# Performance work log

Hardware: AMD Instinct MI355X
Metric: run time of the kernel (lower is better)

## Reference

```python
import jax, jax.numpy as jnp
import numpy as np

N = 50000
IN_CH = 128
HID = 256
HEADS = 8
HEAD_DIM = HID // HEADS
NUM_CLASSES = 2
E = 800000
NEG_SLOPE = 0.2  # PyG GATConv default leaky_relu slope


def gat_conv(x, edge_index, W, att_src, att_dst, bias):
    """PyG-style GATConv (concat=True, add_self_loops=True, eval mode).
    x: [N, HID]; edge_index: [2, E] (row 0 = source j, row 1 = target i).
    W: [HID, HEADS*HEAD_DIM]; att_src/att_dst: [HEADS, HEAD_DIM]; bias: [HEADS*HEAD_DIM].
    """
    loop = jnp.arange(N)
    src = jnp.concatenate([edge_index[0], loop])  # self-loops appended
    dst = jnp.concatenate([edge_index[1], loop])
    h = (x @ W).reshape(N, HEADS, HEAD_DIM)          # [N, H, D]
    a_src = jnp.einsum('nhd,hd->nh', h, att_src)     # [N, H]
    a_dst = jnp.einsum('nhd,hd->nh', h, att_dst)
    e = jax.nn.leaky_relu(a_src[src] + a_dst[dst], NEG_SLOPE)  # [E+N, H]
    # segment softmax over incoming edges of each target node
    m = jax.ops.segment_max(e, dst, num_segments=N)
    p = jnp.exp(e - m[dst])
    s = jax.ops.segment_sum(p, dst, num_segments=N)
    alpha = p / (s[dst] + 1e-16)                     # [E+N, H]
    msg = h[src] * alpha[:, :, None]                 # [E+N, H, D]
    out = jax.ops.segment_sum(msg, dst, num_segments=N)  # [N, H, D]
    return out.reshape(N, HEADS * HEAD_DIM) + bias


def setup_inputs() -> dict:
    key = jax.random.key(0)
    ks = jax.random.split(key, 24)
    g = lambda k, shape, fan_in: jax.random.normal(k, shape, dtype=jnp.float32) / np.sqrt(fan_in)
    inp = {}
    inp['x'] = jax.random.normal(ks[0], (N, IN_CH), dtype=jnp.float32)
    inp['tut_edge_index'] = jax.random.randint(ks[1], (2, E), 0, N)
    inp['tdt_edge_index'] = jax.random.randint(ks[2], (2, E), 0, N)
    inp['proj_W'] = g(ks[3], (IN_CH, HID), IN_CH)
    inp['proj_b'] = jnp.zeros((HID,), jnp.float32)
    # 2 GAT layers per meta-path, stacked on leading axis
    inp['tut_W'] = g(ks[4], (2, HID, HID), HID)
    inp['tut_asrc'] = g(ks[5], (2, HEADS, HEAD_DIM), HEAD_DIM)
    inp['tut_adst'] = g(ks[6], (2, HEADS, HEAD_DIM), HEAD_DIM)
    inp['tut_bias'] = jnp.zeros((2, HID), jnp.float32)
    inp['tdt_W'] = g(ks[7], (2, HID, HID), HID)
    inp['tdt_asrc'] = g(ks[8], (2, HEADS, HEAD_DIM), HEAD_DIM)
    inp['tdt_adst'] = g(ks[9], (2, HEADS, HEAD_DIM), HEAD_DIM)
    inp['tdt_bias'] = jnp.zeros((2, HID), jnp.float32)
    inp['sem_att'] = jnp.full((2,), 0.5, jnp.float32)
    inp['cls_W1'] = g(ks[10], (HID, HID // 2), HID)
    inp['cls_b1'] = jnp.zeros((HID // 2,), jnp.float32)
    inp['cls_W2'] = g(ks[11], (HID // 2, NUM_CLASSES), HID // 2)
    inp['cls_b2'] = jnp.zeros((NUM_CLASSES,), jnp.float32)
    return inp


def reference(x, tut_edge_index, tdt_edge_index, proj_W, proj_b,
              tut_W, tut_asrc, tut_adst, tut_bias,
              tdt_W, tdt_asrc, tdt_adst, tdt_bias,
              sem_att, cls_W1, cls_b1, cls_W2, cls_b2):
    h = x @ proj_W + proj_b
    # TUT branch: 2 GATConv layers (eval mode -> dropout is identity)
    h_tut = h
    for l in range(2):
        h_tut = gat_conv(h_tut, tut_edge_index, tut_W[l], tut_asrc[l], tut_adst[l], tut_bias[l])
        h_tut = jax.nn.elu(h_tut)
    # TDT branch
    h_tdt = h
    for l in range(2):
        h_tdt = gat_conv(h_tdt, tdt_edge_index, tdt_W[l], tdt_asrc[l], tdt_adst[l], tdt_bias[l])
        h_tdt = jax.nn.elu(h_tdt)
    w = jax.nn.softmax(sem_att)
    z = w[0] * h_tut + w[1] * h_tdt
    hc = jax.nn.relu(z @ cls_W1 + cls_b1)
    logits = hc @ cls_W2 + cls_b2  # [N, NUM_CLASSES]
    return logits
```

## Files before the change

### kernel.cpp

```cpp
#include <hip/hip_runtime.h>
#include <hip/hip_fp16.h>
#include <cstddef>
#include <cstdint>


#define HID        256
#define HEADS      8
#define NEG_SLOPE  0.2f
#define ECAP       48

#define BSH     7
#define BNODES  128
#define MAXNB   512
#define CH      2048

typedef __attribute__((ext_vector_type(8))) short short8v;
typedef __attribute__((ext_vector_type(4))) float float4v;

static __device__ __forceinline__ unsigned short f32_to_bf16(float v) {
    union { float f; unsigned u; } c; c.f = v;
    unsigned r = c.u + 0x7FFFu + ((c.u >> 16) & 1u);
    return (unsigned short)(r >> 16);
}
static __device__ __forceinline__ float bf16_to_f32(unsigned short b) {
    union { unsigned u; float f; } c; c.u = ((unsigned)b) << 16;
    return c.f;
}
static __device__ __forceinline__ void split_bf16(float v, unsigned short& hi, unsigned short& lo) {
    hi = f32_to_bf16(v);
    lo = f32_to_bf16(v - bf16_to_f32(hi));
}
static __device__ __forceinline__ void gload_lds16(const void* g, void* l) {
    __builtin_amdgcn_global_load_lds((const __attribute__((address_space(1))) void*)g,
                                     (__attribute__((address_space(3))) void*)l, 16, 0, 0);
}

template<int MODE>
__global__ __launch_bounds__(256) void mfma_gemm_kernel(
    const unsigned short* __restrict__ Ahi, const unsigned short* __restrict__ Alo,
    const unsigned short* __restrict__ Bthi, const unsigned short* __restrict__ Btlo,
    const float* __restrict__ bias,
    unsigned short* __restrict__ Chi, unsigned short* __restrict__ Clo,
    __half* __restrict__ Cf16a, __half* __restrict__ Cf16b, float* __restrict__ Cf32,
    int M, int N, int K)
{
    __shared__ __align__(16) short lds[4 * 4096];

    const int tid  = threadIdx.x;
    const int lane = tid & 63;
    const int w    = tid >> 6;
    const int wr   = w >> 1;
    const int wc   = w & 1;

    const int gx   = gridDim.x;
    const int nwg  = gx * gridDim.y;
    const int flat = blockIdx.y * gx + blockIdx.x;
    const int q    = nwg >> 3, r8 = nwg & 7;
    const int xcd  = flat & 7, idx = flat >> 3;
    const int swz  = (xcd < r8) ? xcd * (q + 1) + idx
                                : r8 * (q + 1) + (xcd - r8) * q + idx;
    const int m0   = (swz / gx) * 128;
    const int n0   = (swz % gx) * 128;

    const unsigned short* sbase = (w == 0) ? Ahi : (w == 1) ? Alo : (w == 2) ? Bthi : Btlo;
    const int rowbase = (w < 2) ? m0 : n0;
    const int rowlim  = ((w < 2) ? M : N) - 1;

    float4v acc[4][4];
    #pragma unroll
    for (int i = 0; i < 4; ++i)
        #pragma unroll
        for (int j = 0; j < 4; ++j)
            acc[i][j] = (float4v){0.f, 0.f, 0.f, 0.f};

    const int kcl = lane >> 4;
    const int rl  = lane & 15;

    for (int k0 = 0; k0 < K; k0 += 32) {
        #pragma unroll
        for (int rh = 0; rh < 2; ++rh) {
            int row = rowbase + rh * 64 + lane;
            row = row > rowlim ? rowlim : row;
            const unsigned short* src = sbase + (size_t)row * K + k0;
            #pragma unroll
            for (int kc = 0; kc < 4; ++kc) {
                short* dst = &lds[w * 4096 + kc * 1024 + rh * 512];
                gload_lds16(src + kc * 8, dst);
            }
        }
        __syncthreads();

        short8v ahi[4], alo[4], bhi[4], blo[4];
        #pragma unroll
        for (int i = 0; i < 4; ++i) {
            int am = wr * 64 + i * 16 + rl;
            int bn = wc * 64 + i * 16 + rl;
            ahi[i] = *(const short8v*)&lds[0 * 4096 + kcl * 1024 + am * 8];
            alo[i] = *(const short8v*)&lds[1 * 4096 + kcl * 1024 + am * 8];
            bhi[i] = *(const short8v*)&lds[2 * 4096 + kcl * 1024 + bn * 8];
            blo[i] = *(const short8v*)&lds[3 * 4096 + kcl * 1024 + bn * 8];
        }
        #pragma unroll
        for (int i = 0; i < 4; ++i)
            #pragma unroll
            for (int j = 0; j < 4; ++j) {
                acc[i][j] = __builtin_amdgcn_mfma_f32_16x16x32_bf16(ahi[i], bhi[j], acc[i][j], 0, 0, 0);
                acc[i][j] = __builtin_amdgcn_mfma_f32_16x16x32_bf16(ahi[i], blo[j], acc[i][j], 0, 0, 0);
                acc[i][j] = __builtin_amdgcn_mfma_f32_16x16x32_bf16(alo[i], bhi[j], acc[i][j], 0, 0, 0);
            }
        __syncthreads();
    }

    const int cr = kcl * 4;
    #pragma unroll
    for (int i = 0; i < 4; ++i) {
        #pragma unroll
        for (int r = 0; r < 4; ++r) {
            int row = m0 + wr * 64 + i * 16 + cr + r;
            if (row >= M) continue;
            #pragma unroll
            for (int j = 0; j < 4; ++j) {
                int col = n0 + wc * 64 + j * 16 + rl;
                float v = acc[i][j][r];
                if (bias) v += bias[col];
                if (MODE == 0) {
                    unsigned short h, l;
                    split_bf16(v, h, l);
                    Chi[(size_t)row * N + col] = h;
                    Clo[(size_t)row * N + col] = l;
                } else if (MODE == 1) {
                    if (col < 256) Cf16a[(size_t)row * 256 + col] = __float2half(v);
                    else           Cf16b[(size_t)row * 256 + (col - 256)] = __float2half(v);
                } else {
                    Cf32[(size_t)row * N + col] = fmaxf(v, 0.f);
                }
            }
        }
    }
}

__global__ void prep_kernel(
    const float* __restrict__ proj_W, const float* __restrict__ tut_W,
    const float* __restrict__ tdt_W, const float* __restrict__ cls_W1,
    unsigned short* __restrict__ pWthi, unsigned short* __restrict__ pWtlo,
    unsigned short* __restrict__ w1hi,  unsigned short* __restrict__ w1lo,
    unsigned short* __restrict__ t2Whi, unsigned short* __restrict__ t2Wlo,
    unsigned short* __restrict__ d2Whi, unsigned short* __restrict__ d2Wlo,
    unsigned short* __restrict__ cWthi, unsigned short* __restrict__ cWtlo,
    const float* __restrict__ x,
    unsigned short* __restrict__ xhi, unsigned short* __restrict__ xlo, int count4x)
{
    const int tid = blockIdx.x * blockDim.x + threadIdx.x;
    const int stride = gridDim.x * blockDim.x;
    for (int idx = tid; idx < 327680; idx += stride) {
        unsigned short h, l;
        if (idx < 32768) {
            int k = idx >> 8, n = idx & 255;
            split_bf16(proj_W[idx], h, l);
            pWthi[n * 128 + k] = h; pWtlo[n * 128 + k] = l;
        } else if (idx < 163840) {
            int r = idx - 32768;
            int ly = r >> 16, rr = r & 65535;
            int k = rr >> 8, n = rr & 255;
            split_bf16(tut_W[r], h, l);
            if (ly == 0) { w1hi[n * 256 + k] = h;  w1lo[n * 256 + k] = l; }
            else         { t2Whi[n * 256 + k] = h; t2Wlo[n * 256 + k] = l; }
        } else if (idx < 294912) {
            int r = idx - 163840;
            int ly = r >> 16, rr = r & 65535;
            int k = rr >> 8, n = rr & 255;
            split_bf16(tdt_W[r], h, l);
            if (ly == 0) { w1hi[(256 + n) * 256 + k] = h; w1lo[(256 + n) * 256 + k] = l; }
            else         { d2Whi[n * 256 + k] = h;        d2Wlo[n * 256 + k] = l; }
        } else {
            int r = idx - 294912;
            int k = r >> 7, n = r & 127;
            split_bf16(cls_W1[r], h, l);
            cWthi[n * 256 + k] = h; cWtlo[n * 256 + k] = l;
        }
    }
    for (int i = tid; i < count4x; i += stride) {
        float4 v = reinterpret_cast<const float4*>(x)[i];
        ushort4 hh, ll;
        split_bf16(v.x, hh.x, ll.x);
        split_bf16(v.y, hh.y, ll.y);
        split_bf16(v.z, hh.z, ll.z);
        split_bf16(v.w, hh.w, ll.w);
        reinterpret_cast<ushort4*>(xhi)[i] = hh;
        reinterpret_cast<ushort4*>(xlo)[i] = ll;
    }
}

__global__ __launch_bounds__(256) void att_kernel(
    const __half* __restrict__ hW,
    const float* __restrict__ att_src, const float* __restrict__ att_dst,
    float* __restrict__ a_src, float* __restrict__ a_dst, int n_nodes)
{
    const int wave = threadIdx.x >> 6;
    const int lane = threadIdx.x & 63;
    const int n = blockIdx.x * 4 + wave;
    if (n >= n_nodes) return;

    const __half2* hp = reinterpret_cast<const __half2*>(&hW[(size_t)n * HID + lane * 4]);
    __half2 h01 = hp[0], h23 = hp[1];
    float hx = __low2float(h01), hy = __high2float(h01);
    float hz = __low2float(h23), hw = __high2float(h23);
    float4 s4 = *reinterpret_cast<const float4*>(&att_src[lane * 4]);
    float4 d4 = *reinterpret_cast<const float4*>(&att_dst[lane * 4]);
    float ps = hx * s4.x + hy * s4.y + hz * s4.z + hw * s4.w;
    float pd = hx * d4.x + hy * d4.y + hz * d4.z + hw * d4.w;
    #pragma unroll
    for (int off = 1; off < 8; off <<= 1) {
        ps += __shfl_xor(ps, off);
        pd += __shfl_xor(pd, off);
    }
    if ((lane & 7) == 0) {
        a_src[n * HEADS + (lane >> 3)] = ps;
        a_dst[n * HEADS + (lane >> 3)] = pd;
    }
}

template<int OMODE>
__global__ __launch_bounds__(256) void gat_kernel(
    const __half* __restrict__ hW,
    const float* __restrict__ a_src, const float* __restrict__ a_dst,
    const int* __restrict__ row_ptr, const int* __restrict__ adj,
    const float* __restrict__ bias,
    const unsigned short* __restrict__ prevHi, const unsigned short* __restrict__ prevLo,
    const float* __restrict__ sem,
    unsigned short* __restrict__ outhi, unsigned short* __restrict__ outlo,
    int n_nodes)
{
    __shared__ float elds_all[4][ECAP * 8];

    const int wave = threadIdx.x >> 6;
    const int lane = threadIdx.x & 63;
    const int n = blockIdx.x * 4 + wave;
    const bool active = (n < n_nodes);
    float* elds = elds_all[wave];

    int beg = 0, end = 0;
    if (active) { beg = row_ptr[n]; end = row_ptr[n + 1]; }
    const int h1 = lane & 7;
    const float adst1 = active ? a_dst[n * HEADS + h1] : 0.f;

    float m = -INFINITY, s = 0.f;
    for (int j = beg + (lane >> 3); j < end; j += 8) {
        float e = a_src[adj[j] * HEADS + h1] + adst1;
        e = (e > 0.f) ? e : NEG_SLOPE * e;
        int jl = j - beg;
        if (jl < ECAP) elds[jl * 8 + h1] = e;
        float mn = fmaxf(m, e);
        float t = (m > -INFINITY) ? s * __expf(m - mn) : 0.f;
        s = t + __expf(e - mn);
        m = mn;
    }
    #pragma unroll
    for (int off = 8; off < 64; off <<= 1) {
        float mo = __shfl_xor(m, off);
        float so = __shfl_xor(s, off);
        float mn = fmaxf(m, mo);
        float t1 = (m  > -INFINITY) ? s  * __expf(m  - mn) : 0.f;
        float t2 = (mo > -INFINITY) ? so * __expf(mo - mn) : 0.f;
        s = t1 + t2;
        m = mn;
    }
    const float inv1 = 1.f / (s + 1e-16f);

    __syncthreads();

    {
        const int cap8 = (active ? ((end - beg < ECAP) ? (end - beg) : ECAP) : 0) * 8;
        for (int idx = lane; idx < cap8; idx += 64)
            elds[idx] = __expf(elds[idx] - m) * inv1;
    }
    __syncthreads();

    const int h2 = lane >> 3;
    const float mh  = __shfl(m, h2);
    const float sh  = __shfl(s, h2);
    const float inv = 1.f / (sh + 1e-16f);
    const float adst2 = active ? a_dst[n * HEADS + h2] : 0.f;
    const int lane4 = lane * 4;

    float4 acc = make_float4(0.f, 0.f, 0.f, 0.f);
    int j = beg;
    for (; j + 4 <= end; j += 4) {
        const int jl = j - beg;
        int s0 = adj[j + 0], s1 = adj[j + 1], s2 = adj[j + 2], s3 = adj[j + 3];
        float al0, al1, al2, al3;
        if (jl + 4 <= ECAP) {
            al0 = elds[(jl + 0) * 8 + h2];
            al1 = elds[(jl + 1) * 8 + h2];
            al2 = elds[(jl + 2) * 8 + h2];
            al3 = elds[(jl + 3) * 8 + h2];
        } else {
            float e0 = a_src[s0 * HEADS + h2] + adst2;
            float e1 = a_src[s1 * HEADS + h2] + adst2;
            float e2 = a_src[s2 * HEADS + h2] + adst2;
            float e3 = a_src[s3 * HEADS + h2] + adst2;
            e0 = (e0 > 0.f) ? e0 : NEG_SLOPE * e0;
            e1 = (e1 > 0.f) ? e1 : NEG_SLOPE * e1;
            e2 = (e2 > 0.f) ? e2 : NEG_SLOPE * e2;
            e3 = (e3 > 0.f) ? e3 : NEG_SLOPE * e3;
            al0 = __expf(e0 - mh) * inv;
            al1 = __expf(e1 - mh) * inv;
            al2 = __expf(e2 - mh) * inv;
            al3 = __expf(e3 - mh) * inv;
        }
        const __half2* p0 = reinterpret_cast<const __half2*>(&hW[(size_t)s0 * HID + lane4]);
        const __half2* p1 = reinterpret_cast<const __half2*>(&hW[(size_t)s1 * HID + lane4]);
        const __half2* p2 = reinterpret_cast<const __half2*>(&hW[(size_t)s2 * HID + lane4]);
        const __half2* p3 = reinterpret_cast<const __half2*>(&hW[(size_t)s3 * HID + lane4]);
        __half2 a01 = p0[0], a23 = p0[1];
        __half2 b01 = p1[0], b23 = p1[1];
        __half2 c01 = p2[0], c23 = p2[1];
        __half2 d01 = p3[0], d23 = p3[1];
        acc.x += al0 * __low2float(a01); acc.y += al0 * __high2float(a01);
        acc.z += al0 * __low2float(a23); acc.w += al0 * __high2float(a23);
        acc.x += al1 * __low2float(b01); acc.y += al1 * __high2float(b01);
        acc.z += al1 * __low2float(b23); acc.w += al1 * __high2float(b23);
        acc.x += al2 * __low2float(c01); acc.y += al2 * __high2float(c01);
        acc.z += al2 * __low2float(c23); acc.w += al2 * __high2float(c23);
        acc.x += al3 * __low2float(d01); acc.y += al3 * __high2float(d01);
        acc.z += al3 * __low2float(d23); acc.w += al3 * __high2float(d23);
    }
    for (; j < end; ++j) {
        const int jl = j - beg;
        int src = adj[j];
        float alpha;
        if (jl < ECAP) {
            alpha = elds[jl * 8 + h2];
        } else {
            float e = a_src[src * HEADS + h2] + adst2;
            e = (e > 0.f) ? e : NEG_SLOPE * e;
            alpha = __expf(e - mh) * inv;
        }
        const __half2* p = reinterpret_cast<const __half2*>(&hW[(size_t)src * HID + lane4]);
        __half2 a01 = p[0], a23 = p[1];
        acc.x += alpha * __low2float(a01); acc.y += alpha * __high2float(a01);
        acc.z += alpha * __low2float(a23); acc.w += alpha * __high2float(a23);
    }

    if (!active) return;

    float4 bv = *reinterpret_cast<const float4*>(&bias[lane4]);
    float4 o;
    o.x = acc.x + bv.x; o.y = acc.y + bv.y; o.z = acc.z + bv.z; o.w = acc.w + bv.w;
    o.x = (o.x > 0.f) ? o.x : expm1f(o.x);
    o.y = (o.y > 0.f) ? o.y : expm1f(o.y);
    o.z = (o.z > 0.f) ? o.z : expm1f(o.z);
    o.w = (o.w > 0.f) ? o.w : expm1f(o.w);

    if (OMODE == 1) {
        const float e0 = __expf(sem[0]);
        const float e1 = __expf(sem[1]);
        const float w0 = e0 / (e0 + e1);
        const float w1 = e1 / (e0 + e1);
        ushort4 ph = *reinterpret_cast<const ushort4*>(&prevHi[(size_t)n * HID + lane4]);
        ushort4 pl = *reinterpret_cast<const ushort4*>(&prevLo[(size_t)n * HID + lane4]);
        o.x = w0 * (bf16_to_f32(ph.x) + bf16_to_f32(pl.x)) + w1 * o.x;
        o.y = w0 * (bf16_to_f32(ph.y) + bf16_to_f32(pl.y)) + w1 * o.y;
        o.z = w0 * (bf16_to_f32(ph.z) + bf16_to_f32(pl.z)) + w1 * o.z;
        o.w = w0 * (bf16_to_f32(ph.w) + bf16_to_f32(pl.w)) + w1 * o.w;
    }

    ushort4 oh, ol;
    split_bf16(o.x, oh.x, ol.x);
    split_bf16(o.y, oh.y, ol.y);
    split_bf16(o.z, oh.z, ol.z);
    split_bf16(o.w, oh.w, ol.w);
    *reinterpret_cast<ushort4*>(&outhi[(size_t)n * HID + lane4]) = oh;
    *reinterpret_cast<ushort4*>(&outlo[(size_t)n * HID + lane4]) = ol;
}

__global__ __launch_bounds__(256) void bucket_count_kernel(
    const int* __restrict__ tut_dst, const int* __restrict__ tdt_dst,
    int* __restrict__ gcount, int E, int NB)
{
    __shared__ int hist[MAXNB];
    const int g = blockIdx.y;
    const int* dstp = g ? tdt_dst : tut_dst;
    for (int i = threadIdx.x; i < MAXNB; i += 256) hist[i] = 0;
    __syncthreads();
    for (int e = blockIdx.x * 256 + threadIdx.x; e < E; e += gridDim.x * 256)
        atomicAdd(&hist[dstp[e] >> BSH], 1);
    __syncthreads();
    for (int i = threadIdx.x; i < NB; i += 256) {
        int c = hist[i];
        if (c) atomicAdd(&gcount[g * NB + i], c);
    }
}

__global__ __launch_bounds__(512) void bucket_scan_kernel(
    const int* __restrict__ gcount, int* __restrict__ ebase, int* __restrict__ adjbase,
    int* __restrict__ rp0, int* __restrict__ rp1, int N, int E, int NB)
{
    __shared__ int sa[MAXNB], sb[MAXNB];
    const int t = threadIdx.x;
    for (int g = 0; g < 2; ++g) {
        int cnt = (t < NB) ? gcount[g * NB + t] : 0;
        int nodes = 0;
        if (t < NB) { int s = t << BSH; nodes = (N - s < BNODES) ? (N - s) : BNODES; }
        sa[t] = cnt;
        sb[t] = cnt + nodes;
        __syncthreads();
        for (int off = 1; off < MAXNB; off <<= 1) {
            int va = (t >= off) ? sa[t - off] : 0;
            int vb = (t >= off) ? sb[t - off] : 0;
            __syncthreads();
            sa[t] += va; sb[t] += vb;
            __syncthreads();
        }
        if (t < NB) {
            ebase[g * (NB + 1) + t + 1] = sa[t];
            adjbase[g * (NB + 1) + t + 1] = sb[t];
        }
        if (t == 0) { ebase[g * (NB + 1)] = 0; adjbase[g * (NB + 1)] = 0; }
        __syncthreads();
    }
    if (t == 0) { rp0[N] = E + N; rp1[N] = E + N; }
}

__global__ __launch_bounds__(256) void bucket_bin_kernel(
    const int* __restrict__ tut_ei, const int* __restrict__ tdt_ei,
    const int* __restrict__ ebase, int* __restrict__ gcursor,
    int* __restrict__ ebuf, int E, int NB)
{
    __shared__ int lhist[MAXNB];
    __shared__ int lbase[MAXNB];
    __shared__ int loffs[MAXNB];
    __shared__ int spair[CH];
    __shared__ int saddr[CH];
    const int g = blockIdx.y;
    const int* ei = g ? tdt_ei : tut_ei;
    const int e0 = blockIdx.x * CH;
    const int cnt = (E - e0 < CH) ? (E - e0) : CH;

    for (int i = threadIdx.x; i < MAXNB; i += 256) lhist[i] = 0;
    __syncthreads();

    int myb[8], myrank[8], mypk[8];
    int nmine = 0;
    #pragma unroll
    for (int k = 0; k < 8; ++k) {
        int idx = e0 + threadIdx.x + k * 256;
        if (idx < e0 + cnt) {
            int sv = ei[idx];
            int dv = ei[E + idx];
            int b = dv >> BSH;
            int r = atomicAdd(&lhist[b], 1);
            myb[nmine] = b; myrank[nmine] = r;
            mypk[nmine] = (sv << BSH) | (dv & (BNODES - 1));
            ++nmine;
        }
    }
    __syncthreads();
    loffs[threadIdx.x] = lhist[threadIdx.x];
    loffs[threadIdx.x + 256] = lhist[threadIdx.x + 256];
    __syncthreads();
    for (int off = 1; off < MAXNB; off <<= 1) {
        int i0 = threadIdx.x, i1 = threadIdx.x + 256;
        int v0 = (i0 >= off) ? loffs[i0 - off] : 0;
        int v1 = (i1 >= off) ? loffs[i1 - off] : 0;
        __syncthreads();
        loffs[i0] += v0; loffs[i1] += v1;
        __syncthreads();
    }
    for (int i = threadIdx.x; i < NB; i += 256) {
        int c = lhist[i];
        lbase[i] = c ? atomicAdd(&gcursor[g * NB + i], c) : 0;
    }
    __syncthreads();
    const int* eb = ebase + g * (NB + 1);
    for (int k = 0; k < nmine; ++k) {
        int b = myb[k];
        int sorted = loffs[b] - lhist[b] + myrank[k];
        spair[sorted] = mypk[k];
        saddr[sorted] = eb[b] + lbase[b] + myrank[k];
    }
    __syncthreads();
    int* out = ebuf + (size_t)g * E;
    for (int i = threadIdx.x; i < cnt; i += 256)
        out[saddr[i]] = spair[i];
}

__global__ __launch_bounds__(256) void bucket_csr_kernel(
    const int* __restrict__ gcount, const int* __restrict__ ebase,
    const int* __restrict__ adjbase, const int* __restrict__ ebuf,
    int* __restrict__ rp0, int* __restrict__ rp1,
    int* __restrict__ adj0, int* __restrict__ adj1, int N, int E, int NB)
{
    __shared__ int hist[BNODES], scn[BNODES], cursor[BNODES];
    const int g = blockIdx.y;
    const int b = blockIdx.x;
    int* rp  = g ? rp1 : rp0;
    int* adj = g ? adj1 : adj0;
    const int cnt = gcount[g * NB + b];
    const int aB  = adjbase[g * (NB + 1) + b];
    const int node0 = b << BSH;
    const int nb = (N - node0 < BNODES) ? (N - node0) : BNODES;
    const int* ep = ebuf + (size_t)g * E + ebase[g * (NB + 1) + b];
    const int t = threadIdx.x;

    if (t < BNODES) hist[t] = 0;
    __syncthreads();
    for (int e = t; e < cnt; e += 256)
        atomicAdd(&hist[ep[e] & (BNODES - 1)], 1);
    __syncthreads();
    if (t < BNODES) scn[t] = (t < nb) ? hist[t] + 1 : 0;
    __syncthreads();
    for (int off = 1; off < BNODES; off <<= 1) {
        int v = 0;
        if (t < BNODES && t >= off) v = scn[t - off];
        __syncthreads();
        if (t < BNODES) scn[t] += v;
        __syncthreads();
    }
    if (t < nb) {
        int s = scn[t] - hist[t] - 1;
        rp[node0 + t] = aB + s;
        adj[aB + s] = node0 + t;
        cursor[t] = s + 1;
    }
    __syncthreads();
    for (int e = t; e < cnt; e += 256) {
        int p = ep[e];
        int pos = atomicAdd(&cursor[p & (BNODES - 1)], 1);
        adj[aB + pos] = p >> BSH;
    }
}

__global__ __launch_bounds__(256) void cls2_kernel(
    const float* __restrict__ hc, const float* __restrict__ W2,
    const float* __restrict__ b2, float* __restrict__ out, int n_nodes)
{
    const int wave = threadIdx.x >> 6;
    const int lane = threadIdx.x & 63;
    const int n = blockIdx.x * 4 + wave;
    if (n >= n_nodes) return;
    float h0 = hc[(size_t)n * 128 + lane];
    float h1 = hc[(size_t)n * 128 + 64 + lane];
    float p0 = h0 * W2[lane * 2 + 0] + h1 * W2[(64 + lane) * 2 + 0];
    float p1 = h0 * W2[lane * 2 + 1] + h1 * W2[(64 + lane) * 2 + 1];
    #pragma unroll
    for (int off = 1; off < 64; off <<= 1) {
        p0 += __shfl_xor(p0, off);
        p1 += __shfl_xor(p1, off);
    }
    if (lane == 0) {
        out[(size_t)n * 2 + 0] = p0 + b2[0];
        out[(size_t)n * 2 + 1] = p1 + b2[1];
    }
}

extern "C" void kernel_launch(void* const* d_in, const int* in_sizes, int n_in,
                              void* d_out, int out_size, void* d_ws, size_t ws_size,
                              hipStream_t stream)
{
    const float* x        = (const float*)d_in[0];
    const int*   tut_ei   = (const int*)d_in[1];
    const int*   tdt_ei   = (const int*)d_in[2];
    const float* proj_W   = (const float*)d_in[3];
    const float* proj_b   = (const float*)d_in[4];
    const float* tut_W    = (const float*)d_in[5];
    const float* tut_asrc = (const float*)d_in[6];
    const float* tut_adst = (const float*)d_in[7];
    const float* tut_bias = (const float*)d_in[8];
    const float* tdt_W    = (const float*)d_in[9];
    const float* tdt_asrc = (const float*)d_in[10];
    const float* tdt_adst = (const float*)d_in[11];
    const float* tdt_bias = (const float*)d_in[12];
    const float* sem_att  = (const float*)d_in[13];
    const float* cls_W1   = (const float*)d_in[14];
    const float* cls_b1   = (const float*)d_in[15];
    const float* cls_W2   = (const float*)d_in[16];
    const float* cls_b2   = (const float*)d_in[17];

    const int IN_CH = 128;
    const int N = in_sizes[0] / IN_CH;
    const int E = in_sizes[1] / 2;
    const int NB = (N + BNODES - 1) >> BSH;
    const size_t NH = (size_t)N * HID;
    const size_t NI = (size_t)N * IN_CH;

    char* base = (char*)d_ws;
    size_t off = 0;
    auto alloc = [&](size_t bytes) -> void* {
        void* p = base + off;
        off = (off + bytes + 255) & ~(size_t)255;
        return p;
    };
    unsigned short* xhi   = (unsigned short*)alloc(NI * 2);
    unsigned short* xlo   = (unsigned short*)alloc(NI * 2);
    unsigned short* t2lo  = (unsigned short*)alloc(NH * 2);
    unsigned short* h0hi  = (unsigned short*)alloc(NH * 2);
    unsigned short* h0lo  = (unsigned short*)alloc(NH * 2);
    unsigned short* l1thi = (unsigned short*)alloc(NH * 2);
    unsigned short* l1tlo = (unsigned short*)alloc(NH * 2);
    __half*         hWa   = (__half*)alloc(NH * 2);
    float* as1 = (float*)alloc((size_t)N * HEADS * sizeof(float));
    float* ad1 = (float*)alloc((size_t)N * HEADS * sizeof(float));
    float* as2 = (float*)alloc((size_t)N * HEADS * sizeof(float));
    float* ad2 = (float*)alloc((size_t)N * HEADS * sizeof(float));
    unsigned short* pWthi = (unsigned short*)alloc(256 * 128 * 2);
    unsigned short* pWtlo = (unsigned short*)alloc(256 * 128 * 2);
    unsigned short* w1hi  = (unsigned short*)alloc(512 * 256 * 2);
    unsigned short* w1lo  = (unsigned short*)alloc(512 * 256 * 2);
    unsigned short* t2Whi = (unsigned short*)alloc(256 * 256 * 2);
    unsigned short* t2Wlo = (unsigned short*)alloc(256 * 256 * 2);
    unsigned short* d2Whi = (unsigned short*)alloc(256 * 256 * 2);
    unsigned short* d2Wlo = (unsigned short*)alloc(256 * 256 * 2);
    unsigned short* cWthi = (unsigned short*)alloc(128 * 256 * 2);
    unsigned short* cWtlo = (unsigned short*)alloc(128 * 256 * 2);
    int* rp_tut  = (int*)alloc((size_t)(N + 1) * sizeof(int));
    int* adj_tut = (int*)alloc((size_t)(E + N) * sizeof(int));
    int* rp_tdt  = (int*)alloc((size_t)(N + 1) * sizeof(int));
    int* adj_tdt = (int*)alloc((size_t)(E + N) * sizeof(int));
    int* gbuf    = (int*)alloc((size_t)4 * NB * sizeof(int));
    int* gcount  = gbuf;
    int* gcursor = gbuf + 2 * NB;
    int* ebase   = (int*)alloc((size_t)2 * (NB + 1) * sizeof(int));
    int* adjbase = (int*)alloc((size_t)2 * (NB + 1) * sizeof(int));
    (void)ws_size; (void)n_in; (void)out_size;

    int* ebuf = (int*)hWa;
    __half* hWb = (__half*)t2lo;
    unsigned short* t2hi = xhi;
    unsigned short* l1dhi = h0hi;
    unsigned short* l1dlo = h0lo;
    unsigned short* zhi = l1thi;
    unsigned short* zlo = l1tlo;
    float* hc = (float*)hWa;

    const int nodeBlocks = (N + 3) / 4;

    hipMemsetAsync(gbuf, 0, (size_t)4 * NB * sizeof(int), stream);
    prep_kernel<<<1024, 256, 0, stream>>>(proj_W, tut_W, tdt_W, cls_W1,
                                          pWthi, pWtlo, w1hi, w1lo, t2Whi, t2Wlo,
                                          d2Whi, d2Wlo, cWthi, cWtlo,
                                          x, xhi, xlo, (int)(NI / 4));
    bucket_count_kernel<<<dim3(128, 2), 256, 0, stream>>>(tut_ei + E, tdt_ei + E, gcount, E, NB);
    bucket_scan_kernel<<<1, 512, 0, stream>>>(gcount, ebase, adjbase, rp_tut, rp_tdt, N, E, NB);
    bucket_bin_kernel<<<dim3((E + CH - 1) / CH, 2), 256, 0, stream>>>(
        tut_ei, tdt_ei, ebase, gcursor, ebuf, E, NB);
    bucket_csr_kernel<<<dim3(NB, 2), 256, 0, stream>>>(
        gcount, ebase, adjbase, ebuf, rp_tut, rp_tdt, adj_tut, adj_tdt, N, E, NB);

    const int gy = (N + 127) / 128;
    const int AS = HEADS * (HID / HEADS);

    mfma_gemm_kernel<0><<<dim3(2, gy), 256, 0, stream>>>(
        xhi, xlo, pWthi, pWtlo, proj_b, h0hi, h0lo, nullptr, nullptr, nullptr,
        N, HID, IN_CH);

    mfma_gemm_kernel<1><<<dim3(4, gy), 256, 0, stream>>>(
        h0hi, h0lo, w1hi, w1lo, nullptr, nullptr, nullptr, hWa, hWb, nullptr,
        N, 512, HID);
    att_kernel<<<nodeBlocks, 256, 0, stream>>>(hWa, tut_asrc, tut_adst, as1, ad1, N);
    att_kernel<<<nodeBlocks, 256, 0, stream>>>(hWb, tdt_asrc, tdt_adst, as2, ad2, N);
    gat_kernel<0><<<nodeBlocks, 256, 0, stream>>>(
        hWa, as1, ad1, rp_tut, adj_tut, tut_bias,
        nullptr, nullptr, nullptr, l1thi, l1tlo, N);
    gat_kernel<0><<<nodeBlocks, 256, 0, stream>>>(
        hWb, as2, ad2, rp_tdt, adj_tdt, tdt_bias,
        nullptr, nullptr, nullptr, l1dhi, l1dlo, N);

    mfma_gemm_kernel<1><<<dim3(2, gy), 256, 0, stream>>>(
        l1thi, l1tlo, t2Whi, t2Wlo, nullptr, nullptr, nullptr, hWa, nullptr, nullptr,
        N, HID, HID);
    att_kernel<<<nodeBlocks, 256, 0, stream>>>(hWa, tut_asrc + AS, tut_adst + AS, as1, ad1, N);
    gat_kernel<0><<<nodeBlocks, 256, 0, stream>>>(
        hWa, as1, ad1, rp_tut, adj_tut, tut_bias + HID,
        nullptr, nullptr, nullptr, t2hi, t2lo, N);

    mfma_gemm_kernel<1><<<dim3(2, gy), 256, 0, stream>>>(
        l1dhi, l1dlo, d2Whi, d2Wlo, nullptr, nullptr, nullptr, hWa, nullptr, nullptr,
        N, HID, HID);
    att_kernel<<<nodeBlocks, 256, 0, stream>>>(hWa, tdt_asrc + AS, tdt_adst + AS, as2, ad2, N);
    gat_kernel<1><<<nodeBlocks, 256, 0, stream>>>(
        hWa, as2, ad2, rp_tdt, adj_tdt, tdt_bias + HID,
        t2hi, t2lo, sem_att, zhi, zlo, N);

    mfma_gemm_kernel<2><<<dim3(1, gy), 256, 0, stream>>>(
        zhi, zlo, cWthi, cWtlo, cls_b1, nullptr, nullptr, nullptr, nullptr, hc,
        N, 128, HID);
    cls2_kernel<<<nodeBlocks, 256, 0, stream>>>(hc, cls_W2, cls_b2, (float*)d_out, N);
}
```

Measured before the change: 709.5 us.

## Fold input projection into first-layer weights and batch second-layer GEMMs

Precomputes proj_W @ [tut_W0 | tdt_W0] (plus a projected bias) with a small GEMM, so the first GAT layer's feature transform runs directly from x with K=128. This removes the N×256 intermediate projection GEMM and its hi/lo bf16 round trip. It also merges the two second-layer GEMMs into one launch using blockIdx.z and reorders the attention and GAT launches to match. The cost is a tiny weight-product kernel and bias kernel per call, and a different rounding path for the fused weights.

```diff
diff --git a/kernel.cpp b/kernel.cpp
--- a/kernel.cpp
+++ b/kernel.cpp
@@ -39,9 +39,12 @@
 __global__ __launch_bounds__(256) void mfma_gemm_kernel(
     const unsigned short* __restrict__ Ahi, const unsigned short* __restrict__ Alo,
     const unsigned short* __restrict__ Bthi, const unsigned short* __restrict__ Btlo,
+    const unsigned short* __restrict__ A2hi, const unsigned short* __restrict__ A2lo,
+    const unsigned short* __restrict__ B2thi, const unsigned short* __restrict__ B2tlo,
     const float* __restrict__ bias,
     unsigned short* __restrict__ Chi, unsigned short* __restrict__ Clo,
-    __half* __restrict__ Cf16a, __half* __restrict__ Cf16b, float* __restrict__ Cf32,
+    __half* __restrict__ Cf16a, __half* __restrict__ Cf16b, __half* __restrict__ Cf16c,
+    float* __restrict__ Cf32,
     int M, int N, int K)
 {
     __shared__ __align__(16) short lds[4 * 4096];
@@ -51,6 +54,13 @@
     const int w    = tid >> 6;
     const int wr   = w >> 1;
     const int wc   = w & 1;
+
+    const bool z1 = (blockIdx.z == 1);
+    const unsigned short* eAhi  = z1 ? A2hi  : Ahi;
+    const unsigned short* eAlo  = z1 ? A2lo  : Alo;
+    const unsigned short* eBthi = z1 ? B2thi : Bthi;
+    const unsigned short* eBtlo = z1 ? B2tlo : Btlo;
+    __half* eCf16a = z1 ? Cf16c : Cf16a;
 
     const int gx   = gridDim.x;
     const int nwg  = gx * gridDim.y;
@@ -62,7 +72,7 @@
     const int m0   = (swz / gx) * 128;
     const int n0   = (swz % gx) * 128;
 
-    const unsigned short* sbase = (w == 0) ? Ahi : (w == 1) ? Alo : (w == 2) ? Bthi : Btlo;
+    const unsigned short* sbase = (w == 0) ? eAhi : (w == 1) ? eAlo : (w == 2) ? eBthi : eBtlo;
     const int rowbase = (w < 2) ? m0 : n0;
     const int rowlim  = ((w < 2) ? M : N) - 1;
 
@@ -123,16 +133,16 @@
                 int col = n0 + wc * 64 + j * 16 + rl;
                 float v = acc[i][j][r];
                 if (bias) v += bias[col];
-                if (MODE == 0) {
+                if (MODE == 1) {
+                    if (col < 256) eCf16a[(size_t)row * 256 + col] = __float2half(v);
+                    else           Cf16b[(size_t)row * 256 + (col - 256)] = __float2half(v);
+                } else if (MODE == 2) {
+                    Cf32[(size_t)row * N + col] = fmaxf(v, 0.f);
+                } else {
                     unsigned short h, l;
                     split_bf16(v, h, l);
-                    Chi[(size_t)row * N + col] = h;
-                    Clo[(size_t)row * N + col] = l;
-                } else if (MODE == 1) {
-                    if (col < 256) Cf16a[(size_t)row * 256 + col] = __float2half(v);
-                    else           Cf16b[(size_t)row * 256 + (col - 256)] = __float2half(v);
-                } else {
-                    Cf32[(size_t)row * N + col] = fmaxf(v, 0.f);
+                    Chi[(size_t)col * M + row] = h;
+                    Clo[(size_t)col * M + row] = l;
                 }
             }
         }
@@ -142,7 +152,7 @@
 __global__ void prep_kernel(
     const float* __restrict__ proj_W, const float* __restrict__ tut_W,
     const float* __restrict__ tdt_W, const float* __restrict__ cls_W1,
-    unsigned short* __restrict__ pWthi, unsigned short* __restrict__ pWtlo,
+    unsigned short* __restrict__ pAhi,  unsigned short* __restrict__ pAlo,
     unsigned short* __restrict__ w1hi,  unsigned short* __restrict__ w1lo,
     unsigned short* __restrict__ t2Whi, unsigned short* __restrict__ t2Wlo,
     unsigned short* __restrict__ d2Whi, unsigned short* __restrict__ d2Wlo,
@@ -155,9 +165,8 @@
     for (int idx = tid; idx < 327680; idx += stride) {
         unsigned short h, l;
         if (idx < 32768) {
-            int k = idx >> 8, n = idx & 255;
             split_bf16(proj_W[idx], h, l);
-            pWthi[n * 128 + k] = h; pWtlo[n * 128 + k] = l;
+            pAhi[idx] = h; pAlo[idx] = l;
         } else if (idx < 163840) {
             int r = idx - 32768;
             int ly = r >> 16, rr = r & 65535;
@@ -189,6 +198,20 @@
         reinterpret_cast<ushort4*>(xhi)[i] = hh;
         reinterpret_cast<ushort4*>(xlo)[i] = ll;
     }
+}
+
+__global__ void bias1_kernel(const float* __restrict__ pb,
+                             const float* __restrict__ tutW,
+                             const float* __restrict__ tdtW,
+                             float* __restrict__ bias1)
+{
+    int n = blockIdx.x * blockDim.x + threadIdx.x;
+    if (n >= 512) return;
+    const float* W = (n < 256) ? tutW : tdtW;
+    int c = n & 255;
+    float s = 0.f;
+    for (int k = 0; k < 256; ++k) s += pb[k] * W[k * 256 + c];
+    bias1[n] = s;
 }
 
 __global__ __launch_bounds__(256) void att_kernel(
@@ -594,19 +617,23 @@
     unsigned short* xhi   = (unsigned short*)alloc(NI * 2);
     unsigned short* xlo   = (unsigned short*)alloc(NI * 2);
     unsigned short* t2lo  = (unsigned short*)alloc(NH * 2);
-    unsigned short* h0hi  = (unsigned short*)alloc(NH * 2);
-    unsigned short* h0lo  = (unsigned short*)alloc(NH * 2);
+    unsigned short* l1dhi = (unsigned short*)alloc(NH * 2);
+    unsigned short* l1dlo = (unsigned short*)alloc(NH * 2);
     unsigned short* l1thi = (unsigned short*)alloc(NH * 2);
     unsigned short* l1tlo = (unsigned short*)alloc(NH * 2);
     __half*         hWa   = (__half*)alloc(NH * 2);
+    __half*         hWc   = (__half*)alloc(NH * 2);
     float* as1 = (float*)alloc((size_t)N * HEADS * sizeof(float));
     float* ad1 = (float*)alloc((size_t)N * HEADS * sizeof(float));
     float* as2 = (float*)alloc((size_t)N * HEADS * sizeof(float));
     float* ad2 = (float*)alloc((size_t)N * HEADS * sizeof(float));
-    unsigned short* pWthi = (unsigned short*)alloc(256 * 128 * 2);
-    unsigned short* pWtlo = (unsigned short*)alloc(256 * 128 * 2);
+    unsigned short* pAhi  = (unsigned short*)alloc(128 * 256 * 2);
+    unsigned short* pAlo  = (unsigned short*)alloc(128 * 256 * 2);
     unsigned short* w1hi  = (unsigned short*)alloc(512 * 256 * 2);
     unsigned short* w1lo  = (unsigned short*)alloc(512 * 256 * 2);
+    unsigned short* cW1thi = (unsigned short*)alloc(512 * 128 * 2);
+    unsigned short* cW1tlo = (unsigned short*)alloc(512 * 128 * 2);
+    float* bias1 = (float*)alloc(512 * sizeof(float));
     unsigned short* t2Whi = (unsigned short*)alloc(256 * 256 * 2);
     unsigned short* t2Wlo = (unsigned short*)alloc(256 * 256 * 2);
     unsigned short* d2Whi = (unsigned short*)alloc(256 * 256 * 2);
@@ -627,19 +654,24 @@
     int* ebuf = (int*)hWa;
     __half* hWb = (__half*)t2lo;
     unsigned short* t2hi = xhi;
-    unsigned short* l1dhi = h0hi;
-    unsigned short* l1dlo = h0lo;
     unsigned short* zhi = l1thi;
     unsigned short* zlo = l1tlo;
     float* hc = (float*)hWa;
 
     const int nodeBlocks = (N + 3) / 4;
+    const int gy = (N + 127) / 128;
+    const int AS = HEADS * (HID / HEADS);
 
     hipMemsetAsync(gbuf, 0, (size_t)4 * NB * sizeof(int), stream);
     prep_kernel<<<1024, 256, 0, stream>>>(proj_W, tut_W, tdt_W, cls_W1,
-                                          pWthi, pWtlo, w1hi, w1lo, t2Whi, t2Wlo,
+                                          pAhi, pAlo, w1hi, w1lo, t2Whi, t2Wlo,
                                           d2Whi, d2Wlo, cWthi, cWtlo,
                                           x, xhi, xlo, (int)(NI / 4));
+    bias1_kernel<<<2, 256, 0, stream>>>(proj_b, tut_W, tdt_W, bias1);
+    mfma_gemm_kernel<3><<<dim3(4, 1), 256, 0, stream>>>(
+        pAhi, pAlo, w1hi, w1lo, nullptr, nullptr, nullptr, nullptr,
+        nullptr, cW1thi, cW1tlo, nullptr, nullptr, nullptr, nullptr,
+        128, 512, 256);
     bucket_count_kernel<<<dim3(128, 2), 256, 0, stream>>>(tut_ei + E, tdt_ei + E, gcount, E, NB);
     bucket_scan_kernel<<<1, 512, 0, stream>>>(gcount, ebase, adjbase, rp_tut, rp_tdt, N, E, NB);
     bucket_bin_kernel<<<dim3((E + CH - 1) / CH, 2), 256, 0, stream>>>(
@@ -647,16 +679,10 @@
     bucket_csr_kernel<<<dim3(NB, 2), 256, 0, stream>>>(
         gcount, ebase, adjbase, ebuf, rp_tut, rp_tdt, adj_tut, adj_tdt, N, E, NB);
 
-    const int gy = (N + 127) / 128;
-    const int AS = HEADS * (HID / HEADS);
-
-    mfma_gemm_kernel<0><<<dim3(2, gy), 256, 0, stream>>>(
-        xhi, xlo, pWthi, pWtlo, proj_b, h0hi, h0lo, nullptr, nullptr, nullptr,
-        N, HID, IN_CH);
-
     mfma_gemm_kernel<1><<<dim3(4, gy), 256, 0, stream>>>(
-        h0hi, h0lo, w1hi, w1lo, nullptr, nullptr, nullptr, hWa, hWb, nullptr,
-        N, 512, HID);
+        xhi, xlo, cW1thi, cW1tlo, nullptr, nullptr, nullptr, nullptr,
+        bias1, nullptr, nullptr, hWa, hWb, nullptr, nullptr,
+        N, 512, 128);
     att_kernel<<<nodeBlocks, 256, 0, stream>>>(hWa, tut_asrc, tut_adst, as1, ad1, N);
     att_kernel<<<nodeBlocks, 256, 0, stream>>>(hWb, tdt_asrc, tdt_adst, as2, ad2, N);
     gat_kernel<0><<<nodeBlocks, 256, 0, stream>>>(
@@ -666,24 +692,22 @@
         hWb, as2, ad2, rp_tdt, adj_tdt, tdt_bias,
         nullptr, nullptr, nullptr, l1dhi, l1dlo, N);
 
-    mfma_gemm_kernel<1><<<dim3(2, gy), 256, 0, stream>>>(
-        l1thi, l1tlo, t2Whi, t2Wlo, nullptr, nullptr, nullptr, hWa, nullptr, nullptr,
+    mfma_gemm_kernel<1><<<dim3(2, gy, 2), 256, 0, stream>>>(
+        l1thi, l1tlo, t2Whi, t2Wlo, l1dhi, l1dlo, d2Whi, d2Wlo,
+        nullptr, nullptr, nullptr, hWa, nullptr, hWc, nullptr,
         N, HID, HID);
     att_kernel<<<nodeBlocks, 256, 0, stream>>>(hWa, tut_asrc + AS, tut_adst + AS, as1, ad1, N);
+    att_kernel<<<nodeBlocks, 256, 0, stream>>>(hWc, tdt_asrc + AS, tdt_adst + AS, as2, ad2, N);
     gat_kernel<0><<<nodeBlocks, 256, 0, stream>>>(
         hWa, as1, ad1, rp_tut, adj_tut, tut_bias + HID,
         nullptr, nullptr, nullptr, t2hi, t2lo, N);
-
-    mfma_gemm_kernel<1><<<dim3(2, gy), 256, 0, stream>>>(
-        l1dhi, l1dlo, d2Whi, d2Wlo, nullptr, nullptr, nullptr, hWa, nullptr, nullptr,
-        N, HID, HID);
-    att_kernel<<<nodeBlocks, 256, 0, stream>>>(hWa, tdt_asrc + AS, tdt_adst + AS, as2, ad2, N);
     gat_kernel<1><<<nodeBlocks, 256, 0, stream>>>(
-        hWa, as2, ad2, rp_tdt, adj_tdt, tdt_bias + HID,
+        hWc, as2, ad2, rp_tdt, adj_tdt, tdt_bias + HID,
         t2hi, t2lo, sem_att, zhi, zlo, N);
 
     mfma_gemm_kernel<2><<<dim3(1, gy), 256, 0, stream>>>(
-        zhi, zlo, cWthi, cWtlo, cls_b1, nullptr, nullptr, nullptr, nullptr, hc,
+        zhi, zlo, cWthi, cWtlo, nullptr, nullptr, nullptr, nullptr,
+        cls_b1, nullptr, nullptr, nullptr, nullptr, nullptr, hc,
         N, 128, HID);
     cls2_kernel<<<nodeBlocks, 256, 0, stream>>>(hc, cls_W2, cls_b2, (float*)d_out, N);
 }
```

Result: faster. 675.8 us (-4.8%).
